# Performance work log

Measured on AMD Instinct MI355X. Metric: run time of the kernel, lower is better.

Reference implementation:

```python
import jax, jax.numpy as jnp
import numpy as np

N_NODES = 100000
IN_FEATS = 512
H_FEATS = 128
N_HOPS = 3
N_NIE = N_HOPS + 1  # 4 per-hop branches
N_EDGES = 1600000


def _layernorm(z, g, b, eps=1e-5):
    mu = jnp.mean(z, axis=-1, keepdims=True)
    var = jnp.var(z, axis=-1, keepdims=True)
    return (z - mu) * jax.lax.rsqrt(var + eps) * g + b


def _mlp(z, W, b, g, be):
    # Dropout(p=0) -> Linear -> LayerNorm -> ReLU (eval mode)
    return jax.nn.relu(_layernorm(z @ W + b, g, be))


def setup_inputs() -> dict:
    key = jax.random.key(0)
    ks = jax.random.split(key, 16)
    ei = jax.random.randint(ks[0], (2, N_EDGES), 0, N_NODES, dtype=jnp.int64)
    feats = jax.random.normal(ks[1], (N_NODES, IN_FEATS), dtype=jnp.float32)
    s_in = 1.0 / np.sqrt(IN_FEATS)
    s_h = 1.0 / np.sqrt(H_FEATS)
    s_c = 1.0 / np.sqrt(N_NIE * H_FEATS)
    return {
        "edge_index": ei,
        "features": feats,
        # unified input transform (transform_first=True): in_feats -> h_feats
        "W_uni": jax.random.normal(ks[2], (IN_FEATS, H_FEATS), jnp.float32) * s_in,
        "b_uni": jnp.zeros((H_FEATS,), jnp.float32),
        "g_uni": jnp.ones((H_FEATS,), jnp.float32),
        "be_uni": jnp.zeros((H_FEATS,), jnp.float32),
        # per-hop independent embeddings: h_feats -> h_feats, one per hop (stacked)
        "W_ind": jax.random.normal(ks[3], (N_NIE, H_FEATS, H_FEATS), jnp.float32) * s_h,
        "b_ind": jnp.zeros((N_NIE, H_FEATS), jnp.float32),
        "g_ind": jnp.ones((N_NIE, H_FEATS), jnp.float32),
        "be_ind": jnp.zeros((N_NIE, H_FEATS), jnp.float32),
        # relation network (RN='concat'): ndim_fc -> h_feats
        "W_rel": jax.random.normal(ks[4], (N_NIE * H_FEATS, H_FEATS), jnp.float32) * s_c,
        "b_rel": jnp.zeros((H_FEATS,), jnp.float32),
        "g_rel": jnp.ones((H_FEATS,), jnp.float32),
        "be_rel": jnp.zeros((H_FEATS,), jnp.float32),
    }


def reference(edge_index, features, W_uni, b_uni, g_uni, be_uni,
              W_ind, b_ind, g_ind, be_ind, W_rel, b_rel, g_rel, be_rel):
    N = features.shape[0]
    # F.normalize(features, dim=1)  (row_normalized=True)
    x = features / jnp.maximum(
        jnp.linalg.norm(features, axis=1, keepdims=True), 1e-12)

    # preprocess_adj: add self loops, then symmetric normalization D^-1/2 A D^-1/2
    loops = jnp.arange(N, dtype=edge_index.dtype)
    row = jnp.concatenate([edge_index[0], loops])
    col = jnp.concatenate([edge_index[1], loops])
    deg = jax.ops.segment_sum(jnp.ones_like(row, dtype=x.dtype), row,
                              num_segments=N)
    dinv = jnp.where(deg > 0, deg ** -0.5, 0.0)
    w = dinv[row] * dinv[col]  # [E+N] edge weights

    def spmm(z):
        # out[row] += w * z[col]   (gather + scatter-add, memory-bound)
        return jax.ops.segment_sum(w[:, None] * z[col], row, num_segments=N)

    # transform_first: unified embedding before multi-hop aggregation
    h = _mlp(x, W_uni, b_uni, g_uni, be_uni)  # [N, H]

    # inceptive aggregation: hop-0 is h itself, hop-i = A^i h; per-hop MLPs
    z = h
    ns = [_mlp(z, W_ind[0], b_ind[0], g_ind[0], be_ind[0])]
    for i in range(1, N_NIE):
        z = spmm(z)
        ns.append(_mlp(z, W_ind[i], b_ind[i], g_ind[i], be_ind[i]))

    cat = jnp.concatenate(ns, axis=1)  # [N, 4*H]
    out = _mlp(cat, W_rel, b_rel, g_rel, be_rel)  # [N, H]
    return out
```

## Files before the change

### kernel.cpp

```cpp
#include <hip/hip_runtime.h>
#include <hip/hip_bf16.h>

#define NN 100000
#define FE 512
#define HF 128
#define NE 1600000
#define NNIE 4

typedef __attribute__((ext_vector_type(8))) __bf16 bf16x8;
typedef __attribute__((ext_vector_type(4))) float f32x4;
typedef __attribute__((ext_vector_type(8))) unsigned short ushort8;

__device__ __forceinline__ unsigned short f2bf(float f) {
    unsigned u = __float_as_uint(f);
    unsigned r = (u + 0x7fffu + ((u >> 16) & 1u)) >> 16;
    return (unsigned short)r;
}
__device__ __forceinline__ float b2f(unsigned short u) {
    return __uint_as_float(((unsigned)u) << 16);
}

__global__ __launch_bounds__(256) void k_zero(int* __restrict__ deg,
                                              int* __restrict__ cursor, int n) {
    int i = blockIdx.x * 256 + threadIdx.x;
    if (i < n) { deg[i] = 0; cursor[i] = 0; }
}

__global__ __launch_bounds__(256) void k_count(const int* __restrict__ row,
                                               int* __restrict__ deg, int e) {
    int i = blockIdx.x * 256 + threadIdx.x;
    if (i < e) atomicAdd(&deg[row[i]], 1);
}

__global__ __launch_bounds__(1024) void k_scan1(const int* __restrict__ cnt,
                                                int* __restrict__ off,
                                                int* __restrict__ bsum,
                                                float* __restrict__ dinv,
                                                int n) {
    __shared__ int wsum[16];
    const int tid = threadIdx.x, lane = tid & 63, wid = tid >> 6;
    const int i = blockIdx.x * 1024 + tid;
    const int v = (i < n) ? cnt[i] : 0;
    if (i < n) dinv[i] = rsqrtf((float)(v + 1));
    int x = v;
#pragma unroll
    for (int s = 1; s < 64; s <<= 1) {
        int t = __shfl_up(x, s);
        if (lane >= s) x += t;
    }
    if (lane == 63) wsum[wid] = x;
    __syncthreads();
    if (wid == 0 && lane < 16) {
        int t = wsum[lane];
#pragma unroll
        for (int s = 1; s < 16; s <<= 1) {
            int u = __shfl_up(t, s);
            if (lane >= s) t += u;
        }
        wsum[lane] = t;
    }
    __syncthreads();
    const int wexc = (wid == 0) ? 0 : wsum[wid - 1];
    if (i < n) off[i] = wexc + x - v;
    if (tid == 0) bsum[blockIdx.x] = wsum[15];
}
__global__ __launch_bounds__(1024) void k_scan2(int* __restrict__ bsum, int nb,
                                                int* __restrict__ total_out) {
    __shared__ int wsum[16];
    const int tid = threadIdx.x, lane = tid & 63, wid = tid >> 6;
    const int v = (tid < nb) ? bsum[tid] : 0;
    int x = v;
#pragma unroll
    for (int s = 1; s < 64; s <<= 1) {
        int t = __shfl_up(x, s);
        if (lane >= s) x += t;
    }
    if (lane == 63) wsum[wid] = x;
    __syncthreads();
    if (wid == 0 && lane < 16) {
        int t = wsum[lane];
#pragma unroll
        for (int s = 1; s < 16; s <<= 1) {
            int u = __shfl_up(t, s);
            if (lane >= s) t += u;
        }
        wsum[lane] = t;
    }
    __syncthreads();
    const int wexc = (wid == 0) ? 0 : wsum[wid - 1];
    if (tid < nb) bsum[tid] = wexc + x - v;
    if (tid == 0) *total_out = wsum[15];
}
__global__ __launch_bounds__(256) void k_scan3(int* __restrict__ off,
                                               const int* __restrict__ bsum,
                                               int n) {
    int i = blockIdx.x * 256 + threadIdx.x;
    if (i < n) off[i] += bsum[i >> 10];
}

__global__ __launch_bounds__(256) void k_fill(const int* __restrict__ rows,
                                              const int* __restrict__ cols,
                                              const float* __restrict__ dinv,
                                              const int* __restrict__ off,
                                              int* __restrict__ cursor,
                                              int2* __restrict__ es, int e) {
    int i = blockIdx.x * 256 + threadIdx.x;
    if (i < e) {
        int r = rows[i], c = cols[i];
        int pos = off[r] + atomicAdd(&cursor[r], 1);
        es[pos] = make_int2(c, __float_as_int(dinv[r] * dinv[c]));
    }
}

__global__ __launch_bounds__(256) void k_wt_all(
    const float* __restrict__ Wu, const float* __restrict__ Wr,
    const float* __restrict__ Wi, unsigned short* __restrict__ Tu,
    unsigned short* __restrict__ Tr, unsigned short* __restrict__ Ti) {
    int i = blockIdx.x * 256 + threadIdx.x;
    if (i < 65536) {
        int k = i >> 7, n = i & 127;
        Tu[n * 512 + k] = f2bf(Wu[i]);
    } else if (i < 131072) {
        int j = i - 65536;
        int k = j >> 7, n = j & 127;
        Tr[n * 512 + k] = f2bf(Wr[j]);
    } else if (i < 196608) {
        int j = i - 131072;
        int hh = j >> 14, r = j & 16383;
        int k = r >> 7, n = r & 127;
        Ti[hh * 16384 + n * 128 + k] = f2bf(Wi[j]);
    }
}

__global__ __launch_bounds__(256) void k_spmm(
    const unsigned short* __restrict__ z, unsigned short* __restrict__ y,
    const int* __restrict__ off, const int2* __restrict__ es,
    const float* __restrict__ dinv, int n) {
    const int node = blockIdx.x * 4 + (threadIdx.x >> 6);
    if (node >= n) return;
    const int lane = threadIdx.x & 63;
    const int g = lane >> 4;
    const int l = lane & 15;

    float acc[8];
#pragma unroll
    for (int j = 0; j < 8; j++) acc[j] = 0.0f;

    const int p0 = off[node], p1 = off[node + 1];
    int p = p0 + g;
    for (; p + 12 < p1; p += 16) {
        const int2 e0 = es[p], e1 = es[p + 4], e2 = es[p + 8], e3 = es[p + 12];
        const ushort8 t0 = *(const ushort8*)(z + (size_t)e0.x * HF + 8 * l);
        const ushort8 t1 = *(const ushort8*)(z + (size_t)e1.x * HF + 8 * l);
        const ushort8 t2 = *(const ushort8*)(z + (size_t)e2.x * HF + 8 * l);
        const ushort8 t3 = *(const ushort8*)(z + (size_t)e3.x * HF + 8 * l);
        const float w0 = __int_as_float(e0.y), w1 = __int_as_float(e1.y);
        const float w2 = __int_as_float(e2.y), w3 = __int_as_float(e3.y);
#pragma unroll
        for (int j = 0; j < 8; j++) acc[j] = fmaf(w0, b2f(t0[j]), acc[j]);
#pragma unroll
        for (int j = 0; j < 8; j++) acc[j] = fmaf(w1, b2f(t1[j]), acc[j]);
#pragma unroll
        for (int j = 0; j < 8; j++) acc[j] = fmaf(w2, b2f(t2[j]), acc[j]);
#pragma unroll
        for (int j = 0; j < 8; j++) acc[j] = fmaf(w3, b2f(t3[j]), acc[j]);
    }
    for (; p + 4 < p1; p += 8) {
        const int2 e0 = es[p], e1 = es[p + 4];
        const ushort8 t0 = *(const ushort8*)(z + (size_t)e0.x * HF + 8 * l);
        const ushort8 t1 = *(const ushort8*)(z + (size_t)e1.x * HF + 8 * l);
        const float w0 = __int_as_float(e0.y), w1 = __int_as_float(e1.y);
#pragma unroll
        for (int j = 0; j < 8; j++) acc[j] = fmaf(w0, b2f(t0[j]), acc[j]);
#pragma unroll
        for (int j = 0; j < 8; j++) acc[j] = fmaf(w1, b2f(t1[j]), acc[j]);
    }
    if (p < p1) {
        const int2 e0 = es[p];
        const ushort8 t0 = *(const ushort8*)(z + (size_t)e0.x * HF + 8 * l);
        const float w0 = __int_as_float(e0.y);
#pragma unroll
        for (int j = 0; j < 8; j++) acc[j] = fmaf(w0, b2f(t0[j]), acc[j]);
    }
    if (g == 0) {
        const float di = dinv[node];
        const ushort8 v = *(const ushort8*)(z + (size_t)node * HF + 8 * l);
        const float d2 = di * di;
#pragma unroll
        for (int j = 0; j < 8; j++) acc[j] = fmaf(d2, b2f(v[j]), acc[j]);
    }
#pragma unroll
    for (int j = 0; j < 8; j++) {
        acc[j] += __shfl_xor(acc[j], 16);
        acc[j] += __shfl_xor(acc[j], 32);
    }
    if (g == 0) {
        ushort8 o;
#pragma unroll
        for (int j = 0; j < 8; j++) o[j] = f2bf(acc[j]);
        *(ushort8*)(y + (size_t)node * HF + 8 * l) = o;
    }
}

__global__ __launch_bounds__(256) void gemm_uni(
    const float* __restrict__ A, const unsigned short* __restrict__ Wt,
    const float* __restrict__ bias, const float* __restrict__ g,
    const float* __restrict__ be, unsigned short* __restrict__ out, int M) {
    constexpr int K = FE;
    constexpr int LDT = 72;
    __shared__ unsigned short Ast[64][LDT];
    __shared__ unsigned short Bst[128][LDT];
    __shared__ float rn_s[64];

    const int tid = threadIdx.x;
    const int row0 = blockIdx.x * 64;
    const int w = tid >> 6;
    const int lane = tid & 63;
    const int m = lane & 15;
    const int q = lane >> 4;
    const int lrow = tid >> 2;
    const int lq = tid & 3;

    f32x4 acc[8];
#pragma unroll
    for (int t = 0; t < 8; t++) acc[t] = (f32x4){0.f, 0.f, 0.f, 0.f};

    float sumsq = 0.0f;
    const bool arow_ok = (row0 + lrow) < M;

    for (int k0 = 0; k0 < K; k0 += 64) {
        __syncthreads();
#pragma unroll
        for (int oo = 0; oo < 2; oo++) {
            const int o = lq + 4 * oo;
            f32x4 a0 = (f32x4){0.f, 0.f, 0.f, 0.f}, a1 = a0;
            if (arow_ok) {
                const float* Ap =
                    A + (size_t)(row0 + lrow) * K + k0 + 8 * o;
                a0 = *(const f32x4*)Ap;
                a1 = *(const f32x4*)(Ap + 4);
            }
#pragma unroll
            for (int j = 0; j < 4; j++) sumsq += a0[j] * a0[j] + a1[j] * a1[j];
            ushort8 pk;
#pragma unroll
            for (int j = 0; j < 4; j++) {
                pk[j] = f2bf(a0[j]);
                pk[j + 4] = f2bf(a1[j]);
            }
            *(ushort8*)&Ast[lrow][8 * o] = pk;
        }
        const int bn = tid >> 1;
#pragma unroll
        for (int kk = 0; kk < 4; kk++) {
            const int o = (tid & 1) + 2 * kk;
            *(ushort8*)&Bst[bn][8 * o] =
                *(const ushort8*)(Wt + (size_t)bn * K + k0 + 8 * o);
        }
        __syncthreads();
#pragma unroll
        for (int jj = 0; jj < 2; jj++) {
            bf16x8 af = *(const bf16x8*)&Ast[16 * w + m][8 * q + 32 * jj];
#pragma unroll
            for (int t = 0; t < 8; t++) {
                bf16x8 bfv = *(const bf16x8*)&Bst[16 * t + m][8 * q + 32 * jj];
                acc[t] = __builtin_amdgcn_mfma_f32_16x16x32_bf16(af, bfv,
                                                                 acc[t], 0, 0,
                                                                 0);
            }
        }
    }

    sumsq += __shfl_xor(sumsq, 1);
    sumsq += __shfl_xor(sumsq, 2);
    if (lq == 0) rn_s[lrow] = 1.0f / fmaxf(sqrtf(sumsq), 1e-12f);
    __syncthreads();

    float bb[8], gg[8], ee[8];
#pragma unroll
    for (int t = 0; t < 8; t++) {
        bb[t] = bias[16 * t + m];
        gg[t] = g[16 * t + m];
        ee[t] = be[16 * t + m];
    }
#pragma unroll
    for (int r = 0; r < 4; r++) {
        const int lrow2 = 16 * w + 4 * q + r;
        const float rn = rn_s[lrow2];
        float s1 = 0.f, s2 = 0.f;
#pragma unroll
        for (int t = 0; t < 8; t++) {
            float y = fmaf(acc[t][r], rn, bb[t]);
            s1 += y;
            s2 = fmaf(y, y, s2);
        }
#pragma unroll
        for (int mask = 1; mask <= 8; mask <<= 1) {
            s1 += __shfl_xor(s1, mask);
            s2 += __shfl_xor(s2, mask);
        }
        const float mean = s1 * (1.0f / 128.0f);
        const float var = fmaxf(s2 * (1.0f / 128.0f) - mean * mean, 0.0f);
        const float rstd = rsqrtf(var + 1e-5f);
        const int grow = row0 + lrow2;
        if (grow < M) {
#pragma unroll
            for (int t = 0; t < 8; t++) {
                float y = fmaf(acc[t][r], rn, bb[t]);
                float o = fmaxf(fmaf((y - mean) * rstd, gg[t], ee[t]), 0.0f);
                out[(size_t)grow * HF + 16 * t + m] = f2bf(o);
            }
        }
    }
}

__global__ __launch_bounds__(256) void k_tail(
    const unsigned short* __restrict__ z0, const unsigned short* __restrict__ z1,
    const unsigned short* __restrict__ z2, const unsigned short* __restrict__ z3,
    const unsigned short* __restrict__ Wt_ind,
    const float* __restrict__ b_ind, const float* __restrict__ g_ind,
    const float* __restrict__ be_ind,
    const unsigned short* __restrict__ Wt_rel,
    const float* __restrict__ b_rel, const float* __restrict__ g_rel,
    const float* __restrict__ be_rel, float* __restrict__ out, int M) {
    constexpr int LDW = 136;
    __shared__ unsigned short Wst[128][LDW];
    __shared__ unsigned short nsT[64][LDW];

    const int tid = threadIdx.x;
    const int row0 = blockIdx.x * 64;
    const int w = tid >> 6;
    const int lane = tid & 63;
    const int m = lane & 15;
    const int q = lane >> 4;
    const int bn = tid >> 1;

    const unsigned short* zs[4] = {z0, z1, z2, z3};

    f32x4 acc2[8];
#pragma unroll
    for (int t = 0; t < 8; t++) acc2[t] = (f32x4){0.f, 0.f, 0.f, 0.f};

    int arow = row0 + 16 * w + m;
    if (arow >= M) arow = M - 1;

#pragma unroll
    for (int hop = 0; hop < NNIE; hop++) {
        __syncthreads();
        const unsigned short* Wi = Wt_ind + hop * HF * HF;
#pragma unroll
        for (int k = 0; k < 8; k++) {
            const int o = (tid & 1) + 2 * k;
            *(ushort8*)&Wst[bn][8 * o] =
                *(const ushort8*)(Wi + (size_t)bn * HF + 8 * o);
        }
        __syncthreads();
        f32x4 acc[8];
#pragma unroll
        for (int t = 0; t < 8; t++) acc[t] = (f32x4){0.f, 0.f, 0.f, 0.f};
        const unsigned short* zp = zs[hop] + (size_t)arow * HF;
#pragma unroll
        for (int jj = 0; jj < 4; jj++) {
            bf16x8 af = *(const bf16x8*)(zp + 8 * q + 32 * jj);
#pragma unroll
            for (int t = 0; t < 8; t++) {
                bf16x8 bfv = *(const bf16x8*)&Wst[16 * t + m][8 * q + 32 * jj];
                acc[t] = __builtin_amdgcn_mfma_f32_16x16x32_bf16(af, bfv,
                                                                 acc[t], 0, 0,
                                                                 0);
            }
        }
        float bb[8], gg[8], ee[8];
#pragma unroll
        for (int t = 0; t < 8; t++) {
            bb[t] = b_ind[hop * HF + 16 * t + m];
            gg[t] = g_ind[hop * HF + 16 * t + m];
            ee[t] = be_ind[hop * HF + 16 * t + m];
        }
#pragma unroll
        for (int r = 0; r < 4; r++) {
            const int lrow2 = 16 * w + 4 * q + r;
            float s1 = 0.f, s2 = 0.f;
#pragma unroll
            for (int t = 0; t < 8; t++) {
                float y = acc[t][r] + bb[t];
                s1 += y;
                s2 = fmaf(y, y, s2);
            }
#pragma unroll
            for (int mask = 1; mask <= 8; mask <<= 1) {
                s1 += __shfl_xor(s1, mask);
                s2 += __shfl_xor(s2, mask);
            }
            const float mean = s1 * (1.0f / 128.0f);
            const float var = fmaxf(s2 * (1.0f / 128.0f) - mean * mean, 0.0f);
            const float rstd = rsqrtf(var + 1e-5f);
#pragma unroll
            for (int t = 0; t < 8; t++) {
                float y = acc[t][r] + bb[t];
                float o = fmaxf(fmaf((y - mean) * rstd, gg[t], ee[t]), 0.0f);
                nsT[lrow2][16 * t + m] = f2bf(o);
            }
        }
        __syncthreads();
#pragma unroll
        for (int k = 0; k < 8; k++) {
            const int o = (tid & 1) + 2 * k;
            *(ushort8*)&Wst[bn][8 * o] =
                *(const ushort8*)(Wt_rel + (size_t)bn * (NNIE * HF) +
                                  HF * hop + 8 * o);
        }
        __syncthreads();
#pragma unroll
        for (int jj = 0; jj < 4; jj++) {
            bf16x8 af = *(const bf16x8*)&nsT[16 * w + m][8 * q + 32 * jj];
#pragma unroll
            for (int t = 0; t < 8; t++) {
                bf16x8 bfv = *(const bf16x8*)&Wst[16 * t + m][8 * q + 32 * jj];
                acc2[t] = __builtin_amdgcn_mfma_f32_16x16x32_bf16(af, bfv,
                                                                  acc2[t], 0,
                                                                  0, 0);
            }
        }
    }

    float bb[8], gg[8], ee[8];
#pragma unroll
    for (int t = 0; t < 8; t++) {
        bb[t] = b_rel[16 * t + m];
        gg[t] = g_rel[16 * t + m];
        ee[t] = be_rel[16 * t + m];
    }
#pragma unroll
    for (int r = 0; r < 4; r++) {
        const int lrow2 = 16 * w + 4 * q + r;
        float s1 = 0.f, s2 = 0.f;
#pragma unroll
        for (int t = 0; t < 8; t++) {
            float y = acc2[t][r] + bb[t];
            s1 += y;
            s2 = fmaf(y, y, s2);
        }
#pragma unroll
        for (int mask = 1; mask <= 8; mask <<= 1) {
            s1 += __shfl_xor(s1, mask);
            s2 += __shfl_xor(s2, mask);
        }
        const float mean = s1 * (1.0f / 128.0f);
        const float var = fmaxf(s2 * (1.0f / 128.0f) - mean * mean, 0.0f);
        const float rstd = rsqrtf(var + 1e-5f);
        const int grow = row0 + lrow2;
        if (grow < M) {
#pragma unroll
            for (int t = 0; t < 8; t++) {
                float y = acc2[t][r] + bb[t];
                float o = fmaxf(fmaf((y - mean) * rstd, gg[t], ee[t]), 0.0f);
                out[(size_t)grow * HF + 16 * t + m] = o;
            }
        }
    }
}

extern "C" void kernel_launch(void* const* d_in, const int* in_sizes, int n_in,
                              void* d_out, int out_size, void* d_ws,
                              size_t ws_size, hipStream_t stream) {
    const int* ei = (const int*)d_in[0];
    const float* feats = (const float*)d_in[1];
    const float* W_uni = (const float*)d_in[2];
    const float* b_uni = (const float*)d_in[3];
    const float* g_uni = (const float*)d_in[4];
    const float* be_uni = (const float*)d_in[5];
    const float* W_ind = (const float*)d_in[6];
    const float* b_ind = (const float*)d_in[7];
    const float* g_ind = (const float*)d_in[8];
    const float* be_ind = (const float*)d_in[9];
    const float* W_rel = (const float*)d_in[10];
    const float* b_rel = (const float*)d_in[11];
    const float* g_rel = (const float*)d_in[12];
    const float* be_rel = (const float*)d_in[13];
    float* out = (float*)d_out;

    char* p = (char*)d_ws;
    auto alloc = [&](size_t bytes) {
        void* r = (void*)p;
        p += (bytes + 255) & ~(size_t)255;
        return r;
    };
    int* deg = (int*)alloc(NN * 4);
    int* cursor = (int*)alloc(NN * 4);
    int* off = (int*)alloc((NN + 1) * 4);
    int* bsum = (int*)alloc(1024 * 4);
    int2* es = (int2*)alloc((size_t)NE * 8);
    float* dinv = (float*)alloc(NN * 4);
    unsigned short* Wt_uni = (unsigned short*)alloc(128 * FE * 2);
    unsigned short* Wt_rel = (unsigned short*)alloc(128 * (NNIE * HF) * 2);
    unsigned short* Wt_ind = (unsigned short*)alloc(NNIE * HF * HF * 2);
    unsigned short* h = (unsigned short*)alloc((size_t)NN * HF * 2);
    unsigned short* za = (unsigned short*)alloc((size_t)NN * HF * 2);
    unsigned short* zb = (unsigned short*)alloc((size_t)NN * HF * 2);
    unsigned short* zc = (unsigned short*)alloc((size_t)NN * HF * 2);

    const int gE = (NE + 255) / 256;
    const int gN = (NN + 255) / 256;
    const int gGemm = (NN + 63) / 64;
    const int gSpmm = (NN + 3) / 4;
    const int nbScan = (NN + 1023) / 1024;
    const int* erow = ei;
    const int* ecol = ei + NE;

    k_zero<<<gN, 256, 0, stream>>>(deg, cursor, NN);
    k_count<<<gE, 256, 0, stream>>>(erow, deg, NE);
    k_scan1<<<nbScan, 1024, 0, stream>>>(deg, off, bsum, dinv, NN);
    k_scan2<<<1, 1024, 0, stream>>>(bsum, nbScan, off + NN);
    k_scan3<<<gN, 256, 0, stream>>>(off, bsum, NN);
    k_fill<<<gE, 256, 0, stream>>>(erow, ecol, dinv, off, cursor, es, NE);

    k_wt_all<<<(196608 + 255) / 256, 256, 0, stream>>>(W_uni, W_rel, W_ind,
                                                       Wt_uni, Wt_rel, Wt_ind);

    gemm_uni<<<gGemm, 256, 0, stream>>>(feats, Wt_uni, b_uni, g_uni, be_uni, h,
                                        NN);
    k_spmm<<<gSpmm, 256, 0, stream>>>(h, za, off, es, dinv, NN);
    k_spmm<<<gSpmm, 256, 0, stream>>>(za, zb, off, es, dinv, NN);
    k_spmm<<<gSpmm, 256, 0, stream>>>(zb, zc, off, es, dinv, NN);

    k_tail<<<gGemm, 256, 0, stream>>>(h, za, zb, zc, Wt_ind, b_ind, g_ind,
                                      be_ind, Wt_rel, b_rel, g_rel, be_rel,
                                      out, NN);
}
```

Measured before the change: 765.4 us.

## Store hidden features in 16-column slices so SpMM gathers hit a compact region

The bf16 hidden activations move from row-major [N,128] to eight feature slices of [N,16]. The SpMM grid becomes eight slices times node chunks, so each block gathers neighbour rows only from one 3.2 MB slice, which improves L2 locality for the random gathers. The producer GEMM and the tail GEMM now write and read this sliced layout. In exchange each gather is 32 bytes instead of 256, so the same index lists are re-read eight times and more blocks are launched.

```diff
diff --git a/kernel.cpp b/kernel.cpp
--- a/kernel.cpp
+++ b/kernel.cpp
@@ -19,6 +19,7 @@
 __device__ __forceinline__ float b2f(unsigned short u) {
     return __uint_as_float(((unsigned)u) << 16);
 }
+
 
 __global__ __launch_bounds__(256) void k_zero(int* __restrict__ deg,
                                               int* __restrict__ cursor, int n) {
@@ -136,39 +137,30 @@
     const unsigned short* __restrict__ z, unsigned short* __restrict__ y,
     const int* __restrict__ off, const int2* __restrict__ es,
     const float* __restrict__ dinv, int n) {
-    const int node = blockIdx.x * 4 + (threadIdx.x >> 6);
+    const int b = blockIdx.x;
+    const int slice = b & 7;
+    const int chunk = b >> 3;
+    const int lane = threadIdx.x & 63;
+    const int waveId = threadIdx.x >> 6;
+    const int ng = lane >> 3;
+    const int sl = (lane >> 1) & 3;
+    const int half = lane & 1;
+    const int node = chunk * 32 + waveId * 8 + ng;
     if (node >= n) return;
-    const int lane = threadIdx.x & 63;
-    const int g = lane >> 4;
-    const int l = lane & 15;
+
+    const unsigned short* zs = z + (size_t)slice * n * 16;
+    unsigned short* ys = y + (size_t)slice * n * 16;
 
     float acc[8];
 #pragma unroll
     for (int j = 0; j < 8; j++) acc[j] = 0.0f;
 
     const int p0 = off[node], p1 = off[node + 1];
-    int p = p0 + g;
-    for (; p + 12 < p1; p += 16) {
-        const int2 e0 = es[p], e1 = es[p + 4], e2 = es[p + 8], e3 = es[p + 12];
-        const ushort8 t0 = *(const ushort8*)(z + (size_t)e0.x * HF + 8 * l);
-        const ushort8 t1 = *(const ushort8*)(z + (size_t)e1.x * HF + 8 * l);
-        const ushort8 t2 = *(const ushort8*)(z + (size_t)e2.x * HF + 8 * l);
-        const ushort8 t3 = *(const ushort8*)(z + (size_t)e3.x * HF + 8 * l);
-        const float w0 = __int_as_float(e0.y), w1 = __int_as_float(e1.y);
-        const float w2 = __int_as_float(e2.y), w3 = __int_as_float(e3.y);
-#pragma unroll
-        for (int j = 0; j < 8; j++) acc[j] = fmaf(w0, b2f(t0[j]), acc[j]);
-#pragma unroll
-        for (int j = 0; j < 8; j++) acc[j] = fmaf(w1, b2f(t1[j]), acc[j]);
-#pragma unroll
-        for (int j = 0; j < 8; j++) acc[j] = fmaf(w2, b2f(t2[j]), acc[j]);
-#pragma unroll
-        for (int j = 0; j < 8; j++) acc[j] = fmaf(w3, b2f(t3[j]), acc[j]);
-    }
+    int p = p0 + sl;
     for (; p + 4 < p1; p += 8) {
         const int2 e0 = es[p], e1 = es[p + 4];
-        const ushort8 t0 = *(const ushort8*)(z + (size_t)e0.x * HF + 8 * l);
-        const ushort8 t1 = *(const ushort8*)(z + (size_t)e1.x * HF + 8 * l);
+        const ushort8 t0 = *(const ushort8*)(zs + (size_t)e0.x * 16 + 8 * half);
+        const ushort8 t1 = *(const ushort8*)(zs + (size_t)e1.x * 16 + 8 * half);
         const float w0 = __int_as_float(e0.y), w1 = __int_as_float(e1.y);
 #pragma unroll
         for (int j = 0; j < 8; j++) acc[j] = fmaf(w0, b2f(t0[j]), acc[j]);
@@ -177,28 +169,28 @@
     }
     if (p < p1) {
         const int2 e0 = es[p];
-        const ushort8 t0 = *(const ushort8*)(z + (size_t)e0.x * HF + 8 * l);
+        const ushort8 t0 = *(const ushort8*)(zs + (size_t)e0.x * 16 + 8 * half);
         const float w0 = __int_as_float(e0.y);
 #pragma unroll
         for (int j = 0; j < 8; j++) acc[j] = fmaf(w0, b2f(t0[j]), acc[j]);
     }
-    if (g == 0) {
+    if (sl == 0) {
         const float di = dinv[node];
-        const ushort8 v = *(const ushort8*)(z + (size_t)node * HF + 8 * l);
+        const ushort8 v = *(const ushort8*)(zs + (size_t)node * 16 + 8 * half);
         const float d2 = di * di;
 #pragma unroll
         for (int j = 0; j < 8; j++) acc[j] = fmaf(d2, b2f(v[j]), acc[j]);
     }
 #pragma unroll
     for (int j = 0; j < 8; j++) {
-        acc[j] += __shfl_xor(acc[j], 16);
-        acc[j] += __shfl_xor(acc[j], 32);
-    }
-    if (g == 0) {
+        acc[j] += __shfl_xor(acc[j], 2);
+        acc[j] += __shfl_xor(acc[j], 4);
+    }
+    if (sl == 0) {
         ushort8 o;
 #pragma unroll
         for (int j = 0; j < 8; j++) o[j] = f2bf(acc[j]);
-        *(ushort8*)(y + (size_t)node * HF + 8 * l) = o;
+        *(ushort8*)(ys + (size_t)node * 16 + 8 * half) = o;
     }
 }
 
@@ -308,7 +300,7 @@
             for (int t = 0; t < 8; t++) {
                 float y = fmaf(acc[t][r], rn, bb[t]);
                 float o = fmaxf(fmaf((y - mean) * rstd, gg[t], ee[t]), 0.0f);
-                out[(size_t)grow * HF + 16 * t + m] = f2bf(o);
+                out[((size_t)t * NN + grow) * 16 + m] = f2bf(o);
             }
         }
     }
@@ -358,10 +350,12 @@
         f32x4 acc[8];
 #pragma unroll
         for (int t = 0; t < 8; t++) acc[t] = (f32x4){0.f, 0.f, 0.f, 0.f};
-        const unsigned short* zp = zs[hop] + (size_t)arow * HF;
+        const unsigned short* zp = zs[hop];
 #pragma unroll
         for (int jj = 0; jj < 4; jj++) {
-            bf16x8 af = *(const bf16x8*)(zp + 8 * q + 32 * jj);
+            bf16x8 af = *(const bf16x8*)(
+                zp + ((size_t)(2 * jj + (q >> 1)) * NN + arow) * 16 +
+                8 * (q & 1));
 #pragma unroll
             for (int t = 0; t < 8; t++) {
                 bf16x8 bfv = *(const bf16x8*)&Wst[16 * t + m][8 * q + 32 * jj];
@@ -503,7 +497,7 @@
     const int gE = (NE + 255) / 256;
     const int gN = (NN + 255) / 256;
     const int gGemm = (NN + 63) / 64;
-    const int gSpmm = (NN + 3) / 4;
+    const int gSpmm = ((NN + 31) / 32) * 8;
     const int nbScan = (NN + 1023) / 1024;
     const int* erow = ei;
     const int* ecol = ei + NE;
```

Result: slower. 834.3 us (+9.0%).
